# Performance work log

Hardware: AMD Instinct MI355X
Metric: run time of the kernel (lower is better)

## Reference

```python
import jax, jax.numpy as jnp
import numpy as np

B, C, T, I, R = 32, 4, 512, 64, 1024
LEAK = 0.5          # reak_rate
DENSITY = 0.1       # reservoir_density
SPECTRAL_RADIUS = 0.95
W_SCALE = 1.0       # reservoir_weights_scale
IN_SCALE = 0.1      # input_weights_scale


def setup_inputs() -> dict:
    rng = np.random.default_rng(0)
    # reservoir weights: uniform, sparsified by density mask, rescaled so the
    # largest singular value equals the target spectral radius (as in __init__)
    W = rng.uniform(-W_SCALE, W_SCALE, (R, R)).astype(np.float32)
    mask = (rng.uniform(0.0, 1.0, (R, R)) < DENSITY).astype(np.float32)
    W = W * mask
    s_max = np.linalg.svd(W, compute_uv=False).max()
    W = W * (SPECTRAL_RADIUS / s_max)
    # input weights: [R, I*C]
    Wi = rng.uniform(-IN_SCALE, IN_SCALE, (R, I * C)).astype(np.float32)

    key = jax.random.key(0)
    x = jax.random.normal(key, (B, C, T, I), dtype=jnp.float32)
    return {
        "x": x,
        "input_weights": jnp.asarray(Wi),
        "reservoir_weights": jnp.asarray(W),
    }


def reference(x, input_weights, reservoir_weights):
    # x: [B, C, T, I]
    B_, C_, T_, I_ = x.shape
    R_ = reservoir_weights.shape[0]
    # precompute the input projection for all steps: u_t = flatten(x[:,:,t,:]) @ Wi.T
    xt = jnp.transpose(x, (2, 0, 1, 3)).reshape(T_, B_, C_ * I_)  # [T, B, C*I]
    U = xt @ input_weights.T                                       # [T, B, R]

    h0 = jnp.zeros((B_, C_, R_), dtype=x.dtype)  # per-channel reservoir state

    def step(h, u):
        # leaky-integrated reservoir update; input broadcasts over channels
        h_new = LEAK * jnp.tanh(u[:, None, :] + h @ reservoir_weights) + (1.0 - LEAK) * h
        return h_new, h_new

    _, hs = jax.lax.scan(step, h0, U)            # hs: [T, B, C, R]
    return jnp.transpose(hs, (1, 2, 0, 3))       # [B, C, T, R]
```

## Files before the change

kernel.cpp:

```cpp
#include <hip/hip_runtime.h>
#include <hip/hip_bf16.h>
#include <cstdint>
#include <cstddef>


typedef unsigned short u16;
typedef unsigned int   u32;
typedef unsigned long long u64;
typedef __bf16 bf16x8 __attribute__((ext_vector_type(8)));
typedef u64    u64x2  __attribute__((ext_vector_type(2)));
typedef float  f32x4  __attribute__((ext_vector_type(4)));
typedef float  f32x2  __attribute__((ext_vector_type(2)));

#define T_STEPS 512
#define NWG     256
#define TPB     256

#define OFF_WHI 0
#define OFF_U   (2*1024*1024)
#define OFF_HB  (OFF_U + (size_t)512*32*1024*4)
#define HB_BYTES ((size_t)128*2048)
#define OFF_BAR (OFF_HB + 2*HB_BYTES)

__device__ __forceinline__ u16 f2bf(float f) {
  u32 u = __builtin_bit_cast(u32, f);
  u += 0x7fffu + ((u >> 16) & 1u);
  return (u16)(u >> 16);
}
__device__ __forceinline__ float bf2f(u16 h) {
  u32 u = ((u32)h) << 16;
  return __builtin_bit_cast(float, u);
}
__device__ __forceinline__ void pinv(bf16x8& v) { asm volatile("" : "+v"(v)); }

__device__ __forceinline__ u32 AADD(u32* p, u32 v) {
  return __hip_atomic_fetch_add(p, v, __ATOMIC_RELAXED, __HIP_MEMORY_SCOPE_AGENT);
}
__device__ __forceinline__ u32 ALD(const u32* p) {
  return __hip_atomic_load(p, __ATOMIC_RELAXED, __HIP_MEMORY_SCOPE_AGENT);
}
__device__ __forceinline__ u64 ALD64(const u64* p) {
  return __hip_atomic_load(p, __ATOMIC_RELAXED, __HIP_MEMORY_SCOPE_AGENT);
}
__device__ __forceinline__ void AST(u32* p, u32 v) {
  __hip_atomic_store(p, v, __ATOMIC_RELAXED, __HIP_MEMORY_SCOPE_AGENT);
}

__global__ void prep_w(const float* __restrict__ W, u16* __restrict__ whi) {
  int n = blockIdx.y;
  int k = blockIdx.x * 256 + threadIdx.x;
  whi[n * 1024 + k] = f2bf(W[k * 1024 + n]);
}

__global__ void __launch_bounds__(256) prep_u2(const float* __restrict__ x,
                                               const float* __restrict__ Wi,
                                               float* __restrict__ U) {
  __shared__ __align__(16) u16 Ah[128 * 128];
  __shared__ __align__(16) u16 Al[128 * 128];
  const int tid = threadIdx.x;
  const int m0 = blockIdx.x << 7;
  const int n0 = blockIdx.y << 7;
  const int wv = tid >> 6, lane = tid & 63;
  const int fc = lane & 15, kb = lane >> 4;

  f32x4 acc[8][2];
#pragma unroll
  for (int mt = 0; mt < 8; ++mt) {
    acc[mt][0] = (f32x4){0.f, 0.f, 0.f, 0.f};
    acc[mt][1] = (f32x4){0.f, 0.f, 0.f, 0.f};
  }

  for (int hf = 0; hf < 2; ++hf) {
    __syncthreads();
#pragma unroll
    for (int s = 0; s < 16; ++s) {
      int f = (s << 8) + tid;
      int row = f >> 5, v = f & 31;
      int cl = v >> 4, i4 = (v & 15) << 2;
      int b = row & 31, t = (m0 + row) >> 5;
      float4 xv = *(const float4*)(x +
          ((size_t)((b << 2) | ((hf << 1) | cl)) * 512 + t) * 64 + i4);
      int byte = (row << 8) + (((cl << 7) + (i4 << 1)) ^ ((row & 7) << 4));
      u16* ph = (u16*)((char*)Ah + byte);
      u16* pl = (u16*)((char*)Al + byte);
      float vv[4] = {xv.x, xv.y, xv.z, xv.w};
#pragma unroll
      for (int e = 0; e < 4; ++e) {
        u16 hh = f2bf(vv[e]);
        ph[e] = hh;
        pl[e] = f2bf(vv[e] - bf2f(hh));
      }
    }
    bf16x8 Bh[2][4], Bl[2][4];
#pragma unroll
    for (int nt = 0; nt < 2; ++nt) {
      const float* wrow = Wi + (size_t)(n0 + (wv << 5) + (nt << 4) + fc) * 256;
#pragma unroll
      for (int kt = 0; kt < 4; ++kt) {
        int k = (hf << 7) + (kt << 5) + (kb << 3);
        float tmp[8];
        *(float4*)&tmp[0] = *(const float4*)(wrow + k);
        *(float4*)&tmp[4] = *(const float4*)(wrow + k + 4);
#pragma unroll
        for (int e = 0; e < 8; ++e) {
          u16 hh = f2bf(tmp[e]);
          Bh[nt][kt][e] = __builtin_bit_cast(__bf16, hh);
          Bl[nt][kt][e] = __builtin_bit_cast(__bf16, f2bf(tmp[e] - bf2f(hh)));
        }
      }
    }
    __syncthreads();
#pragma unroll
    for (int kt = 0; kt < 4; ++kt) {
      int kbyte = (kt << 6) + (kb << 4);
#pragma unroll
      for (int mt = 0; mt < 8; ++mt) {
        int row = (mt << 4) + fc;
        int byte = (row << 8) + (kbyte ^ ((row & 7) << 4));
        bf16x8 ah = *(const bf16x8*)((char*)Ah + byte);
        bf16x8 al = *(const bf16x8*)((char*)Al + byte);
#pragma unroll
        for (int nt = 0; nt < 2; ++nt) {
          acc[mt][nt] = __builtin_amdgcn_mfma_f32_16x16x32_bf16(ah, Bh[nt][kt], acc[mt][nt], 0, 0, 0);
          acc[mt][nt] = __builtin_amdgcn_mfma_f32_16x16x32_bf16(al, Bh[nt][kt], acc[mt][nt], 0, 0, 0);
          acc[mt][nt] = __builtin_amdgcn_mfma_f32_16x16x32_bf16(ah, Bl[nt][kt], acc[mt][nt], 0, 0, 0);
        }
      }
    }
  }
#pragma unroll
  for (int mt = 0; mt < 8; ++mt) {
    int mbase = m0 + (mt << 4) + (kb << 2);
    int n = n0 + (wv << 5) + fc;
#pragma unroll
    for (int nt = 0; nt < 2; ++nt)
#pragma unroll
      for (int r = 0; r < 4; ++r)
        U[(size_t)(mbase + r) * 1024 + n + (nt << 4)] = acc[mt][nt][r];
  }
}

__global__ void __launch_bounds__(TPB, 1) esn_scan(
    const u16* __restrict__ Whi, const float* __restrict__ U,
    u16* __restrict__ Hb, float* __restrict__ out, u32* __restrict__ bar) {
  __shared__ __align__(16) float red[8 * 64 * 4];
  __shared__ int sh_q, sh_j, sh_loc;

  const int tid = threadIdx.x;
  const int wv = tid >> 6, lane = tid & 63;
  const int mcol = lane & 15, kb = lane >> 4;

  if (tid == 0) {
    int xcd;
    asm volatile("s_getreg_b32 %0, hwreg(HW_REG_XCC_ID)" : "=s"(xcd));
    xcd &= 7;
    AADD(bar + xcd * 64, 1u);
    AADD(bar + 512, 1u);
    while (ALD(bar + 512) < (u32)NWG) __builtin_amdgcn_s_sleep(2);
    bool uni = true;
    for (int k = 0; k < 8; ++k) uni &= (ALD(bar + k * 64) == 32u);
    if (uni) {
      sh_q = xcd;
      sh_j = (int)AADD(bar + (9 + xcd) * 64, 1u);
      sh_loc = 1;
    } else {
      sh_q = blockIdx.x & 7;
      sh_j = blockIdx.x >> 3;
      sh_loc = 0;
    }
  }
  __syncthreads();
  const int q = sh_q, j = sh_j;
  const bool xlocal = (sh_loc != 0);
  const int r0 = q << 4, c0 = j << 5;

  bf16x8 bh[2][8];
#pragma unroll
  for (int nt = 0; nt < 2; ++nt) {
    const char* wb = (const char*)Whi + (size_t)(c0 + nt * 16 + mcol) * 2048
                     + wv * 512 + kb * 16;
#pragma unroll
    for (int kt = 0; kt < 8; ++kt)
      bh[nt][kt] = *(const bf16x8*)(wb + kt * 64);
  }
#pragma unroll
  for (int nt = 0; nt < 2; ++nt)
#pragma unroll
    for (int kt = 0; kt < 8; ++kt) pinv(bh[nt][kt]);

  const int row_l = tid >> 4;
  const int col0  = (tid & 15) * 2;
  const int grow  = r0 + row_l;
  const int ont   = col0 >> 4, oci = col0 & 15;
  const int okb   = row_l >> 2, orr = row_l & 3;
  u32* gflags = bar + 2048 + q * 128;
  u32* myslot = gflags + (j << 2) + wv;

  float hreg[2] = {0.f, 0.f};
  float po0 = 0.f, po1 = 0.f;
  f32x2 uf = *(const f32x2*)(U + (size_t)(grow >> 2) * 1024 + c0 + col0);

  for (int t = 0; t < T_STEPS; ++t) {
    const char* hsrc = (const char*)Hb + (size_t)(t & 1) * HB_BYTES
                       + (size_t)(r0 + mcol) * 2048 + wv * 512 + kb * 16;
    bf16x8 av[8];
#pragma unroll
    for (int kt = 0; kt < 8; ++kt)
      av[kt] = *(const bf16x8*)(hsrc + kt * 64);
    f32x2 ufn = uf;
    if (t < T_STEPS - 1)
      ufn = *(const f32x2*)(U + ((size_t)(t + 1) * 32 + (grow >> 2)) * 1024 + c0 + col0);
    __builtin_amdgcn_sched_barrier(0);
    if (t > 0) {
      f32x2 o2; o2.x = po0; o2.y = po1;
      __builtin_nontemporal_store(o2,
          (f32x2*)(out + ((size_t)grow * 512 + (t - 1)) * 1024 + c0 + col0));
    }
    __builtin_amdgcn_sched_barrier(0);

    f32x4 acc0 = {0.f, 0.f, 0.f, 0.f};
    f32x4 acc1 = {0.f, 0.f, 0.f, 0.f};
#pragma unroll
    for (int kt = 0; kt < 8; ++kt) {
      acc0 = __builtin_amdgcn_mfma_f32_16x16x32_bf16(av[kt], bh[0][kt], acc0, 0, 0, 0);
      acc1 = __builtin_amdgcn_mfma_f32_16x16x32_bf16(av[kt], bh[1][kt], acc1, 0, 0, 0);
    }

    *(f32x4*)&red[((wv * 2 + 0) * 64 + lane) * 4] = acc0;
    *(f32x4*)&red[((wv * 2 + 1) * 64 + lane) * 4] = acc1;
    __syncthreads();

    float z0 = 0.f, z1 = 0.f;
#pragma unroll
    for (int w = 0; w < 4; ++w) {
      z0 += red[((w * 2 + ont) * 64 + okb * 16 + oci + 0) * 4 + orr];
      z1 += red[((w * 2 + ont) * 64 + okb * 16 + oci + 1) * 4 + orr];
    }
    float hn0 = 0.5f * tanhf(z0 + uf.x) + 0.5f * hreg[0];
    float hn1 = 0.5f * tanhf(z1 + uf.y) + 0.5f * hreg[1];
    hreg[0] = hn0; hreg[1] = hn1;
    po0 = hn0; po1 = hn1;

    {
      u32 pk = (u32)f2bf(hn0) | ((u32)f2bf(hn1) << 16);
      u32* hdst = (u32*)((char*)Hb + (size_t)((t + 1) & 1) * HB_BYTES
                         + (size_t)grow * 2048 + (c0 + col0) * 2);
      if (xlocal) {
        *hdst = pk;
      } else {
        (void)__hip_atomic_exchange(hdst, pk, __ATOMIC_RELAXED,
                                    __HIP_MEMORY_SCOPE_AGENT);
      }
    }
    asm volatile("s_waitcnt vmcnt(0)" ::: "memory");

    if (t < T_STEPS - 1) {
      if (lane == 0) {
        if (xlocal) *(volatile u32*)myslot = (u32)(t + 1);
        else        AST(myslot, (u32)(t + 1));
      }
      if (wv == 0) {
        u32 tgt = (u32)(t + 1);
        const u32* p0 = gflags + lane;
        const u32* p1 = gflags + 64 + lane;
        if (xlocal) {
          while (true) {
            u32 a = ALD(p0);
            u32 b = ALD(p1);
            if (__all((int)((a >= tgt) & (b >= tgt)))) break;
          }
          asm volatile("buffer_inv\n\ts_waitcnt vmcnt(0)" ::: "memory");
        } else {
          while (true) {
            u32 a = ALD(p0);
            u32 b = ALD(p1);
            if (__all((int)((a >= tgt) & (b >= tgt)))) break;
            __builtin_amdgcn_s_sleep(1);
          }
        }
      }
      __syncthreads();
    }
    uf = ufn;
  }
  {
    f32x2 o2; o2.x = po0; o2.y = po1;
    __builtin_nontemporal_store(o2,
        (f32x2*)(out + ((size_t)grow * 512 + (T_STEPS - 1)) * 1024 + c0 + col0));
  }
}

extern "C" void kernel_launch(void* const* d_in, const int* in_sizes, int n_in,
                              void* d_out, int out_size, void* d_ws, size_t ws_size,
                              hipStream_t stream) {
  (void)in_sizes; (void)n_in; (void)out_size; (void)ws_size;
  const float* x  = (const float*)d_in[0];
  const float* Wi = (const float*)d_in[1];
  const float* W  = (const float*)d_in[2];
  float* out = (float*)d_out;

  char* ws  = (char*)d_ws;
  u16*  whi = (u16*)(ws + OFF_WHI);
  float* U  = (float*)(ws + OFF_U);
  u16*  hb  = (u16*)(ws + OFF_HB);
  u32*  bar = (u32*)(ws + OFF_BAR);

  (void)hipMemsetAsync(ws + OFF_HB, 0, 2 * HB_BYTES + 16384, stream);

  hipLaunchKernelGGL(prep_w, dim3(4, 1024), dim3(256), 0, stream, W, whi);
  hipLaunchKernelGGL(prep_u2, dim3(128, 8), dim3(256), 0, stream, x, Wi, U);
  hipLaunchKernelGGL(esn_scan, dim3(NWG), dim3(TPB), 0, stream,
                     whi, U, hb, out, bar);
}
```

Baseline: 1.499 ms.

## Split the recurrent scan over 512 workgroups with 8-row tiles

```diff
diff --git a/kernel.cpp b/kernel.cpp
--- a/kernel.cpp
+++ b/kernel.cpp
@@ -10,10 +10,9 @@
 typedef __bf16 bf16x8 __attribute__((ext_vector_type(8)));
 typedef u64    u64x2  __attribute__((ext_vector_type(2)));
 typedef float  f32x4  __attribute__((ext_vector_type(4)));
-typedef float  f32x2  __attribute__((ext_vector_type(2)));
 
 #define T_STEPS 512
-#define NWG     256
+#define NWG     512
 #define TPB     256
 
 #define OFF_WHI 0
@@ -140,7 +139,7 @@
   }
 }
 
-__global__ void __launch_bounds__(TPB, 1) esn_scan(
+__global__ void __launch_bounds__(TPB, 2) esn_scan(
     const u16* __restrict__ Whi, const float* __restrict__ U,
     u16* __restrict__ Hb, float* __restrict__ out, u32* __restrict__ bar) {
   __shared__ __align__(16) float red[8 * 64 * 4];
@@ -158,21 +157,22 @@
     AADD(bar + 512, 1u);
     while (ALD(bar + 512) < (u32)NWG) __builtin_amdgcn_s_sleep(2);
     bool uni = true;
-    for (int k = 0; k < 8; ++k) uni &= (ALD(bar + k * 64) == 32u);
+    for (int k = 0; k < 8; ++k) uni &= (ALD(bar + k * 64) == 64u);
     if (uni) {
-      sh_q = xcd;
-      sh_j = (int)AADD(bar + (9 + xcd) * 64, 1u);
+      u32 s = AADD(bar + (9 + xcd) * 64, 1u);
+      sh_q = (xcd << 1) | (int)(s & 1u);
+      sh_j = (int)(s >> 1);
       sh_loc = 1;
     } else {
-      sh_q = blockIdx.x & 7;
-      sh_j = blockIdx.x >> 3;
+      sh_q = blockIdx.x & 15;
+      sh_j = (blockIdx.x >> 4) & 31;
       sh_loc = 0;
     }
   }
   __syncthreads();
   const int q = sh_q, j = sh_j;
   const bool xlocal = (sh_loc != 0);
-  const int r0 = q << 4, c0 = j << 5;
+  const int r0 = q << 3, c0 = j << 5;
 
   bf16x8 bh[2][8];
 #pragma unroll
@@ -188,33 +188,36 @@
 #pragma unroll
     for (int kt = 0; kt < 8; ++kt) pinv(bh[nt][kt]);
 
-  const int row_l = tid >> 4;
-  const int col0  = (tid & 15) * 2;
+  const int row_l = tid >> 5;
+  const int colw  = tid & 31;
   const int grow  = r0 + row_l;
-  const int ont   = col0 >> 4, oci = col0 & 15;
+  const int ont   = colw >> 4, oci = colw & 15;
   const int okb   = row_l >> 2, orr = row_l & 3;
   u32* gflags = bar + 2048 + q * 128;
   u32* myslot = gflags + (j << 2) + wv;
 
-  float hreg[2] = {0.f, 0.f};
-  float po0 = 0.f, po1 = 0.f;
-  f32x2 uf = *(const f32x2*)(U + (size_t)(grow >> 2) * 1024 + c0 + col0);
+  float hreg = 0.f;
+  float po = 0.f;
+  float uf = U[(size_t)(grow >> 2) * 1024 + c0 + colw];
 
   for (int t = 0; t < T_STEPS; ++t) {
     const char* hsrc = (const char*)Hb + (size_t)(t & 1) * HB_BYTES
-                       + (size_t)(r0 + mcol) * 2048 + wv * 512 + kb * 16;
+                       + (size_t)(r0 + (mcol & 7)) * 2048 + wv * 512 + kb * 16;
     bf16x8 av[8];
 #pragma unroll
-    for (int kt = 0; kt < 8; ++kt)
-      av[kt] = *(const bf16x8*)(hsrc + kt * 64);
-    f32x2 ufn = uf;
+    for (int kt = 0; kt < 8; ++kt) {
+      u64x2 p;
+      p.x = ALD64((const u64*)(hsrc + kt * 64));
+      p.y = ALD64((const u64*)(hsrc + kt * 64 + 8));
+      av[kt] = __builtin_bit_cast(bf16x8, p);
+    }
+    float ufn = uf;
     if (t < T_STEPS - 1)
-      ufn = *(const f32x2*)(U + ((size_t)(t + 1) * 32 + (grow >> 2)) * 1024 + c0 + col0);
+      ufn = U[((size_t)(t + 1) * 32 + (grow >> 2)) * 1024 + c0 + colw];
     __builtin_amdgcn_sched_barrier(0);
     if (t > 0) {
-      f32x2 o2; o2.x = po0; o2.y = po1;
-      __builtin_nontemporal_store(o2,
-          (f32x2*)(out + ((size_t)grow * 512 + (t - 1)) * 1024 + c0 + col0));
+      __builtin_nontemporal_store(po,
+          out + ((size_t)grow * 512 + (t - 1)) * 1024 + c0 + colw);
     }
     __builtin_amdgcn_sched_barrier(0);
 
@@ -230,26 +233,26 @@
     *(f32x4*)&red[((wv * 2 + 1) * 64 + lane) * 4] = acc1;
     __syncthreads();
 
-    float z0 = 0.f, z1 = 0.f;
-#pragma unroll
-    for (int w = 0; w < 4; ++w) {
-      z0 += red[((w * 2 + ont) * 64 + okb * 16 + oci + 0) * 4 + orr];
-      z1 += red[((w * 2 + ont) * 64 + okb * 16 + oci + 1) * 4 + orr];
-    }
-    float hn0 = 0.5f * tanhf(z0 + uf.x) + 0.5f * hreg[0];
-    float hn1 = 0.5f * tanhf(z1 + uf.y) + 0.5f * hreg[1];
-    hreg[0] = hn0; hreg[1] = hn1;
-    po0 = hn0; po1 = hn1;
+    float z = 0.f;
+#pragma unroll
+    for (int w = 0; w < 4; ++w)
+      z += red[((w * 2 + ont) * 64 + okb * 16 + oci) * 4 + orr];
+    float hn = 0.5f * tanhf(z + uf) + 0.5f * hreg;
+    hreg = hn;
+    po = hn;
 
     {
-      u32 pk = (u32)f2bf(hn0) | ((u32)f2bf(hn1) << 16);
-      u32* hdst = (u32*)((char*)Hb + (size_t)((t + 1) & 1) * HB_BYTES
-                         + (size_t)grow * 2048 + (c0 + col0) * 2);
+      u16* hdst = (u16*)((char*)Hb + (size_t)((t + 1) & 1) * HB_BYTES
+                         + (size_t)grow * 2048 + (c0 + colw) * 2);
       if (xlocal) {
-        *hdst = pk;
+        *hdst = f2bf(hn);
       } else {
-        (void)__hip_atomic_exchange(hdst, pk, __ATOMIC_RELAXED,
-                                    __HIP_MEMORY_SCOPE_AGENT);
+        float hn_n = __shfl_xor(hn, 1);
+        if ((lane & 1) == 0) {
+          u32 pk = (u32)f2bf(hn) | ((u32)f2bf(hn_n) << 16);
+          (void)__hip_atomic_exchange((u32*)((uintptr_t)hdst & ~3ull), pk,
+                                      __ATOMIC_RELAXED, __HIP_MEMORY_SCOPE_AGENT);
+        }
       }
     }
     asm volatile("s_waitcnt vmcnt(0)" ::: "memory");
@@ -269,7 +272,6 @@
             u32 b = ALD(p1);
             if (__all((int)((a >= tgt) & (b >= tgt)))) break;
           }
-          asm volatile("buffer_inv\n\ts_waitcnt vmcnt(0)" ::: "memory");
         } else {
           while (true) {
             u32 a = ALD(p0);
@@ -283,11 +285,8 @@
     }
     uf = ufn;
   }
-  {
-    f32x2 o2; o2.x = po0; o2.y = po1;
-    __builtin_nontemporal_store(o2,
-        (f32x2*)(out + ((size_t)grow * 512 + (T_STEPS - 1)) * 1024 + c0 + col0));
-  }
+  __builtin_nontemporal_store(po,
+      out + ((size_t)grow * 512 + (T_STEPS - 1)) * 1024 + c0 + colw);
 }
 
 extern "C" void kernel_launch(void* const* d_in, const int* in_sizes, int n_in,
```

After: 3.608 ms. +140.7%, slower.
